# Kernel optimization log

Measured on AMD Instinct MI355X. Metric: run time of the kernel, lower is better.

## Reference

```python
import jax, jax.numpy as jnp
import numpy as np

B, NB, BS, F = 4, 16, 256, 1024   # batch, num_blocks, block_size, features
H, D = 16, 64                     # heads, head_dim
ROPE = 32                         # rope_rotary_dims


def rotate_every_two(x):
    x1 = x[..., ::2]
    x2 = x[..., 1::2]
    return jnp.stack([-x2, x1], axis=-1).reshape(x.shape)


def apply_rope(x, num_blocks, block_size):
    # x: [B, NB, BS, H, rope_dim]
    rope_dim = x.shape[-1]
    inv_freq = 1.0 / 10000.0 ** (jnp.arange(0, rope_dim, 2, dtype=jnp.float32) / rope_dim)
    pos = jnp.arange(num_blocks * block_size, dtype=jnp.float32)
    ang = pos[:, None] * inv_freq[None, :]                       # [S, rope_dim/2]
    sin = jnp.sin(ang).reshape(num_blocks, block_size, rope_dim // 2)
    cos = jnp.cos(ang).reshape(num_blocks, block_size, rope_dim // 2)
    sin = jnp.repeat(sin[None, :, :, None, :], 2, axis=-1)       # [1, NB, BS, 1, rope_dim]
    cos = jnp.repeat(cos[None, :, :, None, :], 2, axis=-1)
    return x * cos + rotate_every_two(x) * sin


def setup_inputs() -> dict:
    key = jax.random.key(0)
    ks = jax.random.split(key, 8)
    s_in = 1.0 / np.sqrt(F)
    s_out = 1.0 / np.sqrt(H * D)
    return {
        "inputs_q": jax.random.normal(ks[0], (B, NB, BS, F), jnp.float32),
        "inputs_kv": jax.random.normal(ks[1], (B, NB, BS, F), jnp.float32),
        "Wq": jax.random.normal(ks[2], (F, H, D), jnp.float32) * s_in,
        "bq": jnp.zeros((H, D), jnp.float32),
        "Wk": jax.random.normal(ks[3], (F, H, D), jnp.float32) * s_in,
        "bk": jnp.zeros((H, D), jnp.float32),
        "Wv": jax.random.normal(ks[4], (F, H, D), jnp.float32) * s_in,
        "bv": jnp.zeros((H, D), jnp.float32),
        "Wo": jax.random.normal(ks[5], (H, D, F), jnp.float32) * s_out,
        "bo": jnp.zeros((F,), jnp.float32),
    }


def reference(inputs_q, inputs_kv, Wq, bq, Wk, bk, Wv, bv, Wo, bo):
    # QKV projections: [B, NB, BS, F] x [F, H, D] -> [B, NB, BS, H, D]
    q = jnp.einsum("bnsf,fhd->bnshd", inputs_q, Wq) + bq
    k = jnp.einsum("bnsf,fhd->bnshd", inputs_kv, Wk) + bk
    v = jnp.einsum("bnsf,fhd->bnshd", inputs_kv, Wv) + bv

    # RoPE on first ROPE dims of head_dim (intended semantics per docstring)
    q_rot, q_pass = q[..., :ROPE], q[..., ROPE:]
    k_rot, k_pass = k[..., :ROPE], k[..., ROPE:]
    q = jnp.concatenate([apply_rope(q_rot, NB, BS), q_pass], axis=-1)
    k = jnp.concatenate([apply_rope(k_rot, NB, BS), k_pass], axis=-1)

    # block-local dot-product attention (flax nn.dot_product_attention semantics)
    q = q / jnp.sqrt(jnp.asarray(D, q.dtype))
    scores = jnp.einsum("bnqhd,bnkhd->bnhqk", q, k)              # [B, NB, H, BS, BS]
    weights = jax.nn.softmax(scores, axis=-1)
    x = jnp.einsum("bnhqk,bnkhd->bnqhd", weights, v)             # [B, NB, BS, H, D]

    # output projection over (heads, head_dim)
    out = jnp.einsum("bnqhd,hdf->bnqf", x, Wo) + bo              # [B, NB, BS, F]
    return out
```

## Files before the change

### kernel.cpp

```cpp
#include <hip/hip_runtime.h>

typedef __attribute__((ext_vector_type(4))) float f32x4;
typedef __attribute__((ext_vector_type(8))) short s16x8;
typedef __attribute__((ext_vector_type(4))) unsigned short u16x4;

struct F2 { float c, s; };

__device__ __forceinline__ unsigned short f2b(float f) {
  unsigned u = __builtin_bit_cast(unsigned, f);
  u += 0x7FFFu + ((u >> 16) & 1u);
  return (unsigned short)(u >> 16);
}
__device__ __forceinline__ void gll16(const void* g, void* l) {
  __builtin_amdgcn_global_load_lds(
      (const __attribute__((address_space(1))) unsigned int*)g,
      (__attribute__((address_space(3))) unsigned int*)l, 16, 0, 0);
}
__device__ __forceinline__ f32x4 mfma16(s16x8 a, s16x8 b, f32x4 c) {
  return __builtin_amdgcn_mfma_f32_16x16x32_bf16(a, b, c, 0, 0, 0);
}

__global__ void k_cvt(const float* __restrict__ src, unsigned short* __restrict__ dst, int n4) {
  int i = blockIdx.x * 256 + threadIdx.x;
  int stride = gridDim.x * 256;
  for (; i < n4; i += stride) {
    f32x4 v = ((const f32x4*)src)[i];
    u16x4 o;
    o.x = f2b(v.x); o.y = f2b(v.y); o.z = f2b(v.z); o.w = f2b(v.w);
    ((u16x4*)dst)[i] = o;
  }
}

__global__ void k_sincos(F2* __restrict__ tab) {
  int idx = blockIdx.x * 256 + threadIdx.x;
  int pos = idx >> 4, fi = idx & 15;
  double inv = exp((double)fi * (-9.210340371976184 / 16.0));
  double a = (double)pos * inv;
  F2 r; r.c = (float)cos(a); r.s = (float)sin(a);
  tab[idx] = r;
}

__global__ void k_transpose(const float* __restrict__ wq,
                            const float* __restrict__ wk,
                            const float* __restrict__ wv,
                            const float* __restrict__ wo,
                            unsigned short* __restrict__ wtqkv,
                            unsigned short* __restrict__ wto) {
  __shared__ unsigned short tile[32][33];
  int z = blockIdx.z;
  const float* src = (z == 0) ? wq : (z == 1) ? wk : (z == 2) ? wv : wo;
  unsigned short* dst = (z < 3) ? (wtqkv + (size_t)z * 1048576) : wto;
  int bx = blockIdx.x * 32, by = blockIdx.y * 32;
  tile[threadIdx.y][threadIdx.x] = f2b(src[(size_t)(by + threadIdx.y) * 1024 + bx + threadIdx.x]);
  __syncthreads();
  dst[(size_t)(bx + threadIdx.y) * 1024 + by + threadIdx.x] = tile[threadIdx.x][threadIdx.y];
}

__global__ __launch_bounds__(256, 2) void k_qkv(
    const unsigned short* __restrict__ Xq,
    const unsigned short* __restrict__ Xkv,
    const unsigned short* __restrict__ WT,
    const float* __restrict__ bq,
    const float* __restrict__ bk,
    const float* __restrict__ bv,
    const F2* __restrict__ tab,
    unsigned short* __restrict__ qbuf,
    unsigned short* __restrict__ kbuf,
    unsigned short* __restrict__ vbuf) {
  __shared__ __align__(16) unsigned short Al[128 * 64];
  __shared__ __align__(16) unsigned short Bl[128 * 64];
  int bid = blockIdx.x;
  int swz = (bid & 7) * 384 + (bid >> 3);
  int mt = swz / 24, nt = swz % 24;
  int m0 = mt * 128, n0 = nt * 128;
  int which = n0 >> 10;
  const unsigned short* X = (which == 0) ? Xq : Xkv;
  const float* bias = (which == 0) ? bq : (which == 1) ? bk : bv;
  unsigned short* dst = (which == 0) ? qbuf : (which == 1) ? kbuf : vbuf;
  int n0l = n0 & 1023;
  int tid = threadIdx.x, wid = tid >> 6, lane = tid & 63;
  int fr = lane & 15, fg = lane >> 4;
  int wr = (wid >> 1) * 64, wc = (wid & 1) * 64;
  int sr = lane >> 3, sc8 = (lane & 7) * 8;

  f32x4 acc[4][4] = {};
  for (int kt = 0; kt < 16; ++kt) {
    int kb = kt * 64;
#pragma unroll
    for (int tt = 0; tt < 4; ++tt) {
      int t = wid * 4 + tt;
      gll16(X  + (size_t)(m0 + t * 8 + sr) * 1024 + kb + sc8, &Al[t * 512]);
      gll16(WT + (size_t)(n0 + t * 8 + sr) * 1024 + kb + sc8, &Bl[t * 512]);
    }
    __syncthreads();
#pragma unroll
    for (int ks = 0; ks < 2; ++ks) {
      int ko = ks * 32 + fg * 8;
      s16x8 af[4], bfr[4];
#pragma unroll
      for (int i = 0; i < 4; ++i) af[i]  = *(const s16x8*)&Al[(wr + i * 16 + fr) * 64 + ko];
#pragma unroll
      for (int i = 0; i < 4; ++i) bfr[i] = *(const s16x8*)&Bl[(wc + i * 16 + fr) * 64 + ko];
#pragma unroll
      for (int mi = 0; mi < 4; ++mi)
#pragma unroll
        for (int ni = 0; ni < 4; ++ni)
          acc[mi][ni] = mfma16(af[mi], bfr[ni], acc[mi][ni]);
    }
    __syncthreads();
  }
#pragma unroll
  for (int mi = 0; mi < 4; ++mi)
#pragma unroll
    for (int ni = 0; ni < 4; ++ni) {
      int c = wc + ni * 16 + fr;
      int col = n0l + c;
      int h = col >> 6, d = col & 63;
      float bz = bias[col];
      bool rope = (which < 2) && (d < 32);
#pragma unroll
      for (int j = 0; j < 4; ++j) {
        int mg = m0 + wr + mi * 16 + fg * 4 + j;
        float v = acc[mi][ni][j] + bz;
        if (rope) {
          float p = __shfl_xor(v, 1);
          F2 cs = tab[(mg & 4095) * 16 + (d >> 1)];
          v = (d & 1) ? fmaf(v, cs.c, p * cs.s) : fmaf(v, cs.c, -(p * cs.s));
        }
        if (which == 0) v *= 0.125f;
        int bn = mg >> 8, s2 = mg & 255;
        dst[((size_t)(bn * 16 + h) * 256 + s2) * 64 + d] = f2b(v);
      }
    }
}

__global__ __launch_bounds__(256, 1) void k_attn(
    const unsigned short* __restrict__ qbuf,
    const unsigned short* __restrict__ kbuf,
    const unsigned short* __restrict__ vbuf,
    unsigned short* __restrict__ xbuf) {
  __shared__ __align__(16) unsigned short Kl[256 * 64];
  __shared__ __align__(16) unsigned short Vt[64 * 264];
  __shared__ __align__(16) unsigned short Pl[4][16 * 264];
  int g = blockIdx.x;
  size_t base = (size_t)g * (256 * 64);
  const unsigned short* Q = qbuf + base;
  const unsigned short* K = kbuf + base;
  const unsigned short* V = vbuf + base;
  int bn = g >> 4, h = g & 15;
  int tid = threadIdx.x, wid = tid >> 6, lane = tid & 63;
  int fr = lane & 15, fg = lane >> 4;

#pragma unroll
  for (int tt = 0; tt < 8; ++tt) {
    int t = wid * 8 + tt;
    int r = t * 8 + (lane >> 3);
    int cp = lane & 7;
    int csrc = cp ^ (r & 7);
    gll16(K + r * 64 + csrc * 8, &Kl[t * 512]);
  }
#pragma unroll
  for (int c8 = 0; c8 < 8; ++c8) {
    s16x8 vv = *(const s16x8*)&V[tid * 64 + c8 * 8];
#pragma unroll
    for (int j = 0; j < 8; ++j)
      Vt[(c8 * 8 + j) * 264 + tid] = (unsigned short)vv[j];
  }
  __syncthreads();

  unsigned short* P = Pl[wid];
  int f7 = fr & 7;
  int c0 = (fg ^ f7) * 8;
  int c1 = ((4 + fg) ^ f7) * 8;
  for (int mtile = 0; mtile < 4; ++mtile) {
    int q0 = wid * 64 + mtile * 16;
    s16x8 qa0 = *(const s16x8*)&Q[(q0 + fr) * 64 + fg * 8];
    s16x8 qa1 = *(const s16x8*)&Q[(q0 + fr) * 64 + 32 + fg * 8];
    f32x4 sc[16] = {};
#pragma unroll
    for (int nt = 0; nt < 16; ++nt) {
      int rr = nt * 16 + fr;
      s16x8 kb0 = *(const s16x8*)&Kl[rr * 64 + c0];
      sc[nt] = mfma16(qa0, kb0, sc[nt]);
      s16x8 kb1 = *(const s16x8*)&Kl[rr * 64 + c1];
      sc[nt] = mfma16(qa1, kb1, sc[nt]);
    }
    float rs[4];
#pragma unroll
    for (int j = 0; j < 4; ++j) {
      float m = sc[0][j];
#pragma unroll
      for (int nt = 1; nt < 16; ++nt) m = fmaxf(m, sc[nt][j]);
      m = fmaxf(m, __shfl_xor(m, 1));
      m = fmaxf(m, __shfl_xor(m, 2));
      m = fmaxf(m, __shfl_xor(m, 4));
      m = fmaxf(m, __shfl_xor(m, 8));
      float sum = 0.f;
#pragma unroll
      for (int nt = 0; nt < 16; ++nt) {
        float p = __expf(sc[nt][j] - m);
        sum += p;
        P[(fg * 4 + j) * 264 + nt * 16 + fr] = f2b(p);
      }
      sum += __shfl_xor(sum, 1);
      sum += __shfl_xor(sum, 2);
      sum += __shfl_xor(sum, 4);
      sum += __shfl_xor(sum, 8);
      rs[j] = 1.0f / sum;
    }
    f32x4 o[4] = {};
#pragma unroll
    for (int ks = 0; ks < 8; ++ks) {
      s16x8 pa = *(const s16x8*)&P[fr * 264 + ks * 32 + fg * 8];
#pragma unroll
      for (int nt = 0; nt < 4; ++nt) {
        s16x8 vb = *(const s16x8*)&Vt[(nt * 16 + fr) * 264 + ks * 32 + fg * 8];
        o[nt] = mfma16(pa, vb, o[nt]);
      }
    }
#pragma unroll
    for (int nt = 0; nt < 4; ++nt)
#pragma unroll
      for (int j = 0; j < 4; ++j) {
        int srow = q0 + fg * 4 + j;
        int d = nt * 16 + fr;
        xbuf[((size_t)(bn * 256 + srow)) * 1024 + h * 64 + d] = f2b(o[nt][j] * rs[j]);
      }
  }
}

__global__ __launch_bounds__(256, 2) void k_out(
    const unsigned short* __restrict__ Xb,
    const unsigned short* __restrict__ WT,
    const float* __restrict__ bo,
    float* __restrict__ out) {
  __shared__ __align__(16) unsigned short Al[128 * 64];
  __shared__ __align__(16) unsigned short Bl[128 * 64];
  int bid = blockIdx.x;
  int swz = (bid & 7) * 128 + (bid >> 3);
  int mt = swz >> 3, nt = swz & 7;
  int m0 = mt * 128, n0 = nt * 128;
  int tid = threadIdx.x, wid = tid >> 6, lane = tid & 63;
  int fr = lane & 15, fg = lane >> 4;
  int wr = (wid >> 1) * 64, wc = (wid & 1) * 64;
  int sr = lane >> 3, sc8 = (lane & 7) * 8;
  f32x4 acc[4][4] = {};
  for (int kt = 0; kt < 16; ++kt) {
    int kb = kt * 64;
#pragma unroll
    for (int tt = 0; tt < 4; ++tt) {
      int t = wid * 4 + tt;
      gll16(Xb + (size_t)(m0 + t * 8 + sr) * 1024 + kb + sc8, &Al[t * 512]);
      gll16(WT + (size_t)(n0 + t * 8 + sr) * 1024 + kb + sc8, &Bl[t * 512]);
    }
    __syncthreads();
#pragma unroll
    for (int ks = 0; ks < 2; ++ks) {
      int ko = ks * 32 + fg * 8;
      s16x8 af[4], bfr[4];
#pragma unroll
      for (int i = 0; i < 4; ++i) af[i]  = *(const s16x8*)&Al[(wr + i * 16 + fr) * 64 + ko];
#pragma unroll
      for (int i = 0; i < 4; ++i) bfr[i] = *(const s16x8*)&Bl[(wc + i * 16 + fr) * 64 + ko];
#pragma unroll
      for (int mi = 0; mi < 4; ++mi)
#pragma unroll
        for (int ni = 0; ni < 4; ++ni)
          acc[mi][ni] = mfma16(af[mi], bfr[ni], acc[mi][ni]);
    }
    __syncthreads();
  }
#pragma unroll
  for (int mi = 0; mi < 4; ++mi)
#pragma unroll
    for (int ni = 0; ni < 4; ++ni) {
      int c = wc + ni * 16 + fr;
      float bz = bo[n0 + c];
#pragma unroll
      for (int j = 0; j < 4; ++j) {
        int mg = m0 + wr + mi * 16 + fg * 4 + j;
        out[(size_t)mg * 1024 + n0 + c] = acc[mi][ni][j] + bz;
      }
    }
}

extern "C" void kernel_launch(void* const* d_in, const int* in_sizes, int n_in,
                              void* d_out, int out_size, void* d_ws, size_t ws_size,
                              hipStream_t stream) {
  const float* Xq  = (const float*)d_in[0];
  const float* Xkv = (const float*)d_in[1];
  const float* Wq  = (const float*)d_in[2];
  const float* bq  = (const float*)d_in[3];
  const float* Wk  = (const float*)d_in[4];
  const float* bk  = (const float*)d_in[5];
  const float* Wv  = (const float*)d_in[6];
  const float* bv  = (const float*)d_in[7];
  const float* Wo  = (const float*)d_in[8];
  const float* bo  = (const float*)d_in[9];
  float* out = (float*)d_out;

  char* ws = (char*)d_ws;
  size_t off = 0;
  F2* tab = (F2*)(ws + off);                           off += (size_t)65536 * sizeof(F2);
  unsigned short* WTqkv = (unsigned short*)(ws + off); off += (size_t)3 * 1048576 * 2;
  unsigned short* WTo   = (unsigned short*)(ws + off); off += (size_t)1048576 * 2;
  unsigned short* Xqb   = (unsigned short*)(ws + off); off += (size_t)16777216 * 2;
  unsigned short* Xkvb  = (unsigned short*)(ws + off); off += (size_t)16777216 * 2;
  unsigned short* qb = (unsigned short*)(ws + off); off += (size_t)16777216 * 2;
  unsigned short* kb = (unsigned short*)(ws + off); off += (size_t)16777216 * 2;
  unsigned short* vb = (unsigned short*)(ws + off); off += (size_t)16777216 * 2;
  unsigned short* xb = Xqb;

  k_cvt<<<2048, 256, 0, stream>>>(Xq,  Xqb,  4194304);
  k_cvt<<<2048, 256, 0, stream>>>(Xkv, Xkvb, 4194304);
  k_sincos<<<256, 256, 0, stream>>>(tab);
  k_transpose<<<dim3(32, 32, 4), dim3(32, 32), 0, stream>>>(Wq, Wk, Wv, Wo, WTqkv, WTo);
  k_qkv<<<3072, 256, 0, stream>>>(Xqb, Xkvb, WTqkv, bq, bk, bv, tab, qb, kb, vb);
  k_attn<<<1024, 256, 0, stream>>>(qb, kb, vb, xb);
  k_out<<<1024, 256, 0, stream>>>(xb, WTo, bo, out);
}
```

Baseline: 290.0 us.

## Rewrite QKV and output GEMMs with 256x128 tiles and triple-buffered LDS pipeline

Both projection GEMMs move to 512-thread blocks with 256x128 output tiles and a three-stage LDS ring, prefetching two K-steps ahead. Each step uses a single barrier, with explicit vmcnt waits in place of two syncthreads. LDS tiles are XOR-swizzled to avoid bank conflicts, and s_setprio raises priority during the MFMA sections. This aims to hide global-load latency and cut barrier overhead, in exchange for 144KB LDS per block (one block per CU) and higher register pressure from 8x2 accumulators.

```diff
diff --git a/kernel.cpp b/kernel.cpp
--- a/kernel.cpp
+++ b/kernel.cpp
@@ -56,7 +56,7 @@
   dst[(size_t)(bx + threadIdx.y) * 1024 + by + threadIdx.x] = tile[threadIdx.x][threadIdx.y];
 }
 
-__global__ __launch_bounds__(256, 2) void k_qkv(
+__global__ __launch_bounds__(512, 1) void k_qkv(
     const unsigned short* __restrict__ Xq,
     const unsigned short* __restrict__ Xkv,
     const unsigned short* __restrict__ WT,
@@ -67,12 +67,11 @@
     unsigned short* __restrict__ qbuf,
     unsigned short* __restrict__ kbuf,
     unsigned short* __restrict__ vbuf) {
-  __shared__ __align__(16) unsigned short Al[128 * 64];
-  __shared__ __align__(16) unsigned short Bl[128 * 64];
+  __shared__ __align__(16) unsigned short S[3][24576];
   int bid = blockIdx.x;
-  int swz = (bid & 7) * 384 + (bid >> 3);
+  int swz = (bid & 7) * 192 + (bid >> 3);
   int mt = swz / 24, nt = swz % 24;
-  int m0 = mt * 128, n0 = nt * 128;
+  int m0 = mt * 256, n0 = nt * 128;
   int which = n0 >> 10;
   const unsigned short* X = (which == 0) ? Xq : Xkv;
   const float* bias = (which == 0) ? bq : (which == 1) ? bk : bv;
@@ -80,48 +79,74 @@
   int n0l = n0 & 1023;
   int tid = threadIdx.x, wid = tid >> 6, lane = tid & 63;
   int fr = lane & 15, fg = lane >> 4;
-  int wr = (wid >> 1) * 64, wc = (wid & 1) * 64;
-  int sr = lane >> 3, sc8 = (lane & 7) * 8;
-
-  f32x4 acc[4][4] = {};
-  for (int kt = 0; kt < 16; ++kt) {
-    int kb = kt * 64;
-#pragma unroll
-    for (int tt = 0; tt < 4; ++tt) {
-      int t = wid * 4 + tt;
-      gll16(X  + (size_t)(m0 + t * 8 + sr) * 1024 + kb + sc8, &Al[t * 512]);
-      gll16(WT + (size_t)(n0 + t * 8 + sr) * 1024 + kb + sc8, &Bl[t * 512]);
-    }
-    __syncthreads();
+  int wm = wid >> 2, wn = wid & 3;
+  int l8 = lane >> 3, g = lane & 7;
+
+  f32x4 acc[8][2] = {};
+
+  auto STAGE = [&](int t) {
+    int kb = t * 64;
+    unsigned short* sa = &S[t % 3][0];
+    unsigned short* sb = sa + 16384;
+#pragma unroll
+    for (int c = 0; c < 4; ++c) {
+      int q = wid * 4 + c;
+      int row = q * 8 + l8;
+      gll16(X + (size_t)(m0 + row) * 1024 + kb + (g ^ (row & 7)) * 8, sa + q * 512);
+    }
+#pragma unroll
+    for (int c = 0; c < 2; ++c) {
+      int q = wid * 2 + c;
+      int row = q * 8 + l8;
+      gll16(WT + (size_t)(n0 + row) * 1024 + kb + (g ^ (row & 7)) * 8, sb + q * 512);
+    }
+  };
+
+  STAGE(0);
+  STAGE(1);
+  int rx = fr & 7;
+  for (int t = 0; t < 16; ++t) {
+    if (t < 15) asm volatile("s_waitcnt vmcnt(6)" ::: "memory");
+    else        asm volatile("s_waitcnt vmcnt(0)" ::: "memory");
+    __builtin_amdgcn_sched_barrier(0);
+    __builtin_amdgcn_s_barrier();
+    __builtin_amdgcn_sched_barrier(0);
+    if (t + 2 < 16) STAGE(t + 2);
+    const unsigned short* sa = &S[t % 3][0];
+    const unsigned short* sb = sa + 16384;
+    __builtin_amdgcn_s_setprio(1);
 #pragma unroll
     for (int ks = 0; ks < 2; ++ks) {
-      int ko = ks * 32 + fg * 8;
-      s16x8 af[4], bfr[4];
-#pragma unroll
-      for (int i = 0; i < 4; ++i) af[i]  = *(const s16x8*)&Al[(wr + i * 16 + fr) * 64 + ko];
-#pragma unroll
-      for (int i = 0; i < 4; ++i) bfr[i] = *(const s16x8*)&Bl[(wc + i * 16 + fr) * 64 + ko];
-#pragma unroll
-      for (int mi = 0; mi < 4; ++mi)
-#pragma unroll
-        for (int ni = 0; ni < 4; ++ni)
-          acc[mi][ni] = mfma16(af[mi], bfr[ni], acc[mi][ni]);
-    }
-    __syncthreads();
-  }
-#pragma unroll
-  for (int mi = 0; mi < 4; ++mi)
-#pragma unroll
-    for (int ni = 0; ni < 4; ++ni) {
-      int c = wc + ni * 16 + fr;
-      int col = n0l + c;
-      int h = col >> 6, d = col & 63;
-      float bz = bias[col];
-      bool rope = (which < 2) && (d < 32);
+      int gsw = ((ks * 4 + fg) ^ rx) * 8;
+      s16x8 af[8], bf2[2];
+#pragma unroll
+      for (int mf = 0; mf < 8; ++mf)
+        af[mf] = *(const s16x8*)&sa[(wm * 128 + mf * 16 + fr) * 64 + gsw];
+#pragma unroll
+      for (int nf = 0; nf < 2; ++nf)
+        bf2[nf] = *(const s16x8*)&sb[(wn * 32 + nf * 16 + fr) * 64 + gsw];
+#pragma unroll
+      for (int mf = 0; mf < 8; ++mf)
+#pragma unroll
+        for (int nf = 0; nf < 2; ++nf)
+          acc[mf][nf] = mfma16(af[mf], bf2[nf], acc[mf][nf]);
+    }
+    __builtin_amdgcn_s_setprio(0);
+  }
+
+#pragma unroll
+  for (int nf = 0; nf < 2; ++nf) {
+    int c = wn * 32 + nf * 16 + fr;
+    int col = n0l + c;
+    int h = col >> 6, d = col & 63;
+    float bz = bias[col];
+    bool rope = (which < 2) && (d < 32);
+#pragma unroll
+    for (int mf = 0; mf < 8; ++mf) {
 #pragma unroll
       for (int j = 0; j < 4; ++j) {
-        int mg = m0 + wr + mi * 16 + fg * 4 + j;
-        float v = acc[mi][ni][j] + bz;
+        int mg = m0 + wm * 128 + mf * 16 + fg * 4 + j;
+        float v = acc[mf][nf][j] + bz;
         if (rope) {
           float p = __shfl_xor(v, 1);
           F2 cs = tab[(mg & 4095) * 16 + (d >> 1)];
@@ -132,6 +157,7 @@
         dst[((size_t)(bn * 16 + h) * 256 + s2) * 64 + d] = f2b(v);
       }
     }
+  }
 }
 
 __global__ __launch_bounds__(256, 1) void k_attn(
@@ -142,12 +168,12 @@
   __shared__ __align__(16) unsigned short Kl[256 * 64];
   __shared__ __align__(16) unsigned short Vt[64 * 264];
   __shared__ __align__(16) unsigned short Pl[4][16 * 264];
-  int g = blockIdx.x;
-  size_t base = (size_t)g * (256 * 64);
+  int gb = blockIdx.x;
+  size_t base = (size_t)gb * (256 * 64);
   const unsigned short* Q = qbuf + base;
   const unsigned short* K = kbuf + base;
   const unsigned short* V = vbuf + base;
-  int bn = g >> 4, h = g & 15;
+  int bn = gb >> 4, h = gb & 15;
   int tid = threadIdx.x, wid = tid >> 6, lane = tid & 63;
   int fr = lane & 15, fg = lane >> 4;
 
@@ -229,59 +255,86 @@
   }
 }
 
-__global__ __launch_bounds__(256, 2) void k_out(
+__global__ __launch_bounds__(512, 1) void k_out(
     const unsigned short* __restrict__ Xb,
     const unsigned short* __restrict__ WT,
     const float* __restrict__ bo,
     float* __restrict__ out) {
-  __shared__ __align__(16) unsigned short Al[128 * 64];
-  __shared__ __align__(16) unsigned short Bl[128 * 64];
+  __shared__ __align__(16) unsigned short S[3][24576];
   int bid = blockIdx.x;
-  int swz = (bid & 7) * 128 + (bid >> 3);
+  int swz = (bid & 7) * 64 + (bid >> 3);
   int mt = swz >> 3, nt = swz & 7;
-  int m0 = mt * 128, n0 = nt * 128;
+  int m0 = mt * 256, n0 = nt * 128;
   int tid = threadIdx.x, wid = tid >> 6, lane = tid & 63;
   int fr = lane & 15, fg = lane >> 4;
-  int wr = (wid >> 1) * 64, wc = (wid & 1) * 64;
-  int sr = lane >> 3, sc8 = (lane & 7) * 8;
-  f32x4 acc[4][4] = {};
-  for (int kt = 0; kt < 16; ++kt) {
-    int kb = kt * 64;
-#pragma unroll
-    for (int tt = 0; tt < 4; ++tt) {
-      int t = wid * 4 + tt;
-      gll16(Xb + (size_t)(m0 + t * 8 + sr) * 1024 + kb + sc8, &Al[t * 512]);
-      gll16(WT + (size_t)(n0 + t * 8 + sr) * 1024 + kb + sc8, &Bl[t * 512]);
-    }
-    __syncthreads();
+  int wm = wid >> 2, wn = wid & 3;
+  int l8 = lane >> 3, g = lane & 7;
+
+  f32x4 acc[8][2] = {};
+
+  auto STAGE = [&](int t) {
+    int kb = t * 64;
+    unsigned short* sa = &S[t % 3][0];
+    unsigned short* sb = sa + 16384;
+#pragma unroll
+    for (int c = 0; c < 4; ++c) {
+      int q = wid * 4 + c;
+      int row = q * 8 + l8;
+      gll16(Xb + (size_t)(m0 + row) * 1024 + kb + (g ^ (row & 7)) * 8, sa + q * 512);
+    }
+#pragma unroll
+    for (int c = 0; c < 2; ++c) {
+      int q = wid * 2 + c;
+      int row = q * 8 + l8;
+      gll16(WT + (size_t)(n0 + row) * 1024 + kb + (g ^ (row & 7)) * 8, sb + q * 512);
+    }
+  };
+
+  STAGE(0);
+  STAGE(1);
+  int rx = fr & 7;
+  for (int t = 0; t < 16; ++t) {
+    if (t < 15) asm volatile("s_waitcnt vmcnt(6)" ::: "memory");
+    else        asm volatile("s_waitcnt vmcnt(0)" ::: "memory");
+    __builtin_amdgcn_sched_barrier(0);
+    __builtin_amdgcn_s_barrier();
+    __builtin_amdgcn_sched_barrier(0);
+    if (t + 2 < 16) STAGE(t + 2);
+    const unsigned short* sa = &S[t % 3][0];
+    const unsigned short* sb = sa + 16384;
+    __builtin_amdgcn_s_setprio(1);
 #pragma unroll
     for (int ks = 0; ks < 2; ++ks) {
-      int ko = ks * 32 + fg * 8;
-      s16x8 af[4], bfr[4];
-#pragma unroll
-      for (int i = 0; i < 4; ++i) af[i]  = *(const s16x8*)&Al[(wr + i * 16 + fr) * 64 + ko];
-#pragma unroll
-      for (int i = 0; i < 4; ++i) bfr[i] = *(const s16x8*)&Bl[(wc + i * 16 + fr) * 64 + ko];
-#pragma unroll
-      for (int mi = 0; mi < 4; ++mi)
-#pragma unroll
-        for (int ni = 0; ni < 4; ++ni)
-          acc[mi][ni] = mfma16(af[mi], bfr[ni], acc[mi][ni]);
-    }
-    __syncthreads();
-  }
-#pragma unroll
-  for (int mi = 0; mi < 4; ++mi)
-#pragma unroll
-    for (int ni = 0; ni < 4; ++ni) {
-      int c = wc + ni * 16 + fr;
-      float bz = bo[n0 + c];
+      int gsw = ((ks * 4 + fg) ^ rx) * 8;
+      s16x8 af[8], bf2[2];
+#pragma unroll
+      for (int mf = 0; mf < 8; ++mf)
+        af[mf] = *(const s16x8*)&sa[(wm * 128 + mf * 16 + fr) * 64 + gsw];
+#pragma unroll
+      for (int nf = 0; nf < 2; ++nf)
+        bf2[nf] = *(const s16x8*)&sb[(wn * 32 + nf * 16 + fr) * 64 + gsw];
+#pragma unroll
+      for (int mf = 0; mf < 8; ++mf)
+#pragma unroll
+        for (int nf = 0; nf < 2; ++nf)
+          acc[mf][nf] = mfma16(af[mf], bf2[nf], acc[mf][nf]);
+    }
+    __builtin_amdgcn_s_setprio(0);
+  }
+
+#pragma unroll
+  for (int nf = 0; nf < 2; ++nf) {
+    int c = wn * 32 + nf * 16 + fr;
+    float bz = bo[n0 + c];
+#pragma unroll
+    for (int mf = 0; mf < 8; ++mf) {
 #pragma unroll
       for (int j = 0; j < 4; ++j) {
-        int mg = m0 + wr + mi * 16 + fg * 4 + j;
-        out[(size_t)mg * 1024 + n0 + c] = acc[mi][ni][j] + bz;
-      }
-    }
+        int mg = m0 + wm * 128 + mf * 16 + fg * 4 + j;
+        out[(size_t)mg * 1024 + n0 + c] = acc[mf][nf][j] + bz;
+      }
+    }
+  }
 }
 
 extern "C" void kernel_launch(void* const* d_in, const int* in_sizes, int n_in,
@@ -315,7 +368,7 @@
   k_cvt<<<2048, 256, 0, stream>>>(Xkv, Xkvb, 4194304);
   k_sincos<<<256, 256, 0, stream>>>(tab);
   k_transpose<<<dim3(32, 32, 4), dim3(32, 32), 0, stream>>>(Wq, Wk, Wv, Wo, WTqkv, WTo);
-  k_qkv<<<3072, 256, 0, stream>>>(Xqb, Xkvb, WTqkv, bq, bk, bv, tab, qb, kb, vb);
+  k_qkv<<<1536, 512, 0, stream>>>(Xqb, Xkvb, WTqkv, bq, bk, bv, tab, qb, kb, vb);
   k_attn<<<1024, 256, 0, stream>>>(qb, kb, vb, xb);
-  k_out<<<1024, 256, 0, stream>>>(xb, WTo, bo, out);
-}
+  k_out<<<512, 512, 0, stream>>>(xb, WTo, bo, out);
+}
```

Measured after the change: 344.2 us. +18.7%, slower.
